# Performance work log

Measured on AMD Instinct MI355X. Metric: run time of the kernel, lower is better.

## Reference

```python
import jax, jax.numpy as jnp
import numpy as np

NUM_HEADS = 16
EMB = 1024
HEAD = 64
SEQ = 2048
BATCH = 4


def setup_inputs() -> dict:
    key = jax.random.key(0)
    ks = jax.random.split(key, 6)
    s = EMB ** -0.5
    x = jax.random.normal(ks[0], (BATCH, SEQ, EMB), dtype=jnp.float32)
    # per-head projection weights stacked: [H, E, D] (Linear(emb, head, bias=False) per head)
    Wq = jax.random.normal(ks[1], (NUM_HEADS, EMB, HEAD), dtype=jnp.float32) * s
    Wk = jax.random.normal(ks[2], (NUM_HEADS, EMB, HEAD), dtype=jnp.float32) * s
    Wv = jax.random.normal(ks[3], (NUM_HEADS, EMB, HEAD), dtype=jnp.float32) * s
    # output projection Linear(head*num_heads, emb): weight [E, H*D], bias [E]
    Wo = jax.random.normal(ks[4], (EMB, NUM_HEADS * HEAD), dtype=jnp.float32) * ((NUM_HEADS * HEAD) ** -0.5)
    bo = jax.random.normal(ks[5], (EMB,), dtype=jnp.float32) * 0.01
    return {"x": x, "Wq": Wq, "Wk": Wk, "Wv": Wv, "Wo": Wo, "bo": bo}


def reference(x, Wq, Wk, Wv, Wo, bo):
    B, S, E = x.shape
    scale = HEAD ** -0.5
    # batched per-head projections: [B, H, S, D]
    q = jnp.einsum('bse,hed->bhsd', x, Wq)
    k = jnp.einsum('bse,hed->bhsd', x, Wk)
    v = jnp.einsum('bse,hed->bhsd', x, Wv)
    scores = jnp.einsum('bhqd,bhkd->bhqk', q, k) * scale
    causal = jnp.tril(jnp.ones((S, S), dtype=bool))
    scores = jnp.where(causal, scores, jnp.finfo(scores.dtype).min)
    attn = jax.nn.softmax(scores, axis=-1)  # dropout disabled (eval/deterministic)
    ctx = jnp.einsum('bhqk,bhkd->bhqd', attn, v)
    # concat heads along last dim (head-major order, matching torch.cat)
    concat = ctx.transpose(0, 2, 1, 3).reshape(B, S, NUM_HEADS * HEAD)
    out = concat @ Wo.T + bo
    return out
```

## Files before the change

kernel.cpp:

```cpp
#include <hip/hip_runtime.h>

#define NHEADS 16
#define EMB 1024
#define HDIM 64
#define SEQ 2048
#define BATCH 4

typedef unsigned short u16;
typedef __attribute__((ext_vector_type(8))) __bf16 bf16x8;
typedef __attribute__((ext_vector_type(4))) float f32x4;

#if __has_builtin(__builtin_amdgcn_exp2f)
#define EXP2(x) __builtin_amdgcn_exp2f(x)
#else
#define EXP2(x) __expf((x)*0.69314718056f)
#endif
#define CL2E 0.18033688011112042f

#define BARRIER() __builtin_amdgcn_s_barrier()
#define SB0() __builtin_amdgcn_sched_barrier(0)
#define PRIO1() __builtin_amdgcn_s_setprio(1)
#define PRIO0() __builtin_amdgcn_s_setprio(0)
#define VMCNT(n) asm volatile("s_waitcnt vmcnt(" #n ")" ::: "memory")

__device__ __forceinline__ u16 f2bf(float f) {
  union { float f; unsigned u; } v; v.f = f;
  unsigned r = v.u + 0x7fffu + ((v.u >> 16) & 1u);
  return (u16)(r >> 16);
}
__device__ __forceinline__ unsigned pk2bf(float a, float b) {
  union { __bf16 h[2]; unsigned u; } x;
  x.h[0] = (__bf16)a; x.h[1] = (__bf16)b; return x.u;
}
__device__ __forceinline__ void gl16(const void* g, void* l) {
  __builtin_amdgcn_global_load_lds(
      (const __attribute__((address_space(1))) unsigned*)g,
      (__attribute__((address_space(3))) unsigned*)l, 16, 0, 0);
}

__global__ __launch_bounds__(256) void k_cvt(const float* __restrict__ in,
                                             u16* __restrict__ out, int n4) {
  int i = blockIdx.x * 256 + threadIdx.x;
  if (i >= n4) return;
  f32x4 v = *(const f32x4*)(in + (size_t)i * 4);
  uint2 o;
  o.x = (unsigned)f2bf(v[0]) | ((unsigned)f2bf(v[1]) << 16);
  o.y = (unsigned)f2bf(v[2]) | ((unsigned)f2bf(v[3]) << 16);
  *(uint2*)(out + (size_t)i * 4) = o;
}

__global__ __launch_bounds__(256) void k_packw(const float* __restrict__ Wq,
                                               const float* __restrict__ Wk,
                                               const float* __restrict__ Wv,
                                               u16* __restrict__ Wt) {
  const int mh = blockIdx.x;
  const int e0 = blockIdx.y * 64;
  const int mtx = mh >> 4, h = mh & 15;
  const float* W = (mtx == 0 ? Wq : (mtx == 1 ? Wk : Wv)) + (size_t)h * EMB * HDIM;
  __shared__ u16 sT[64][65];
  const int t = threadIdx.x;
  {
    int e = t >> 2, d0 = (t & 3) * 16;
#pragma unroll
    for (int jj = 0; jj < 4; jj++) {
      f32x4 v = *(const f32x4*)(W + (size_t)(e0 + e) * HDIM + d0 + jj * 4);
#pragma unroll
      for (int kk = 0; kk < 4; kk++) sT[e][d0 + jj * 4 + kk] = f2bf(v[kk]);
    }
  }
  __syncthreads();
  {
    int d = t >> 2, eb = (t & 3) * 16;
#pragma unroll
    for (int j = 0; j < 16; j++)
      Wt[(size_t)(mh * 64 + d) * EMB + e0 + eb + j] = sT[eb + j][d];
  }
}

__global__ __launch_bounds__(512, 2) void k_gemm_qkv8(const u16* __restrict__ Xb,
                                                      const u16* __restrict__ Wt,
                                                      u16* __restrict__ Q,
                                                      u16* __restrict__ K,
                                                      u16* __restrict__ V) {
  extern __shared__ __align__(16) char smem[];
  const int bid = blockIdx.x;
  const int l = (bid & 7) * 64 + (bid >> 3);
  const int mt = l & 31, nt = l >> 5;
  const int m0 = mt * 256, n0 = nt * 192;

  const int t = threadIdx.x;
  const int wave = t >> 6, lane = t & 63, lr = lane & 15, lg = lane >> 4;
  const int wr = (wave >> 2) * 128;
  const int wc = (wave & 3) * 48;

  const f32x4 fz = {0.f, 0.f, 0.f, 0.f};
  f32x4 acc[8][3];
#pragma unroll
  for (int i = 0; i < 8; i++)
#pragma unroll
    for (int j = 0; j < 3; j++) acc[i][j] = fz;

  bf16x8 af[4][2], bfr[3][2];

  auto SROUND = [&](char* ldsbase, int rbase, const u16* src, int gRowBase, int kt) {
    int rs = rbase + wave * 8;
    int row = rs + (lane >> 3);
    int gc = (lane & 7) ^ (row & 7);
    gl16(src + (size_t)(gRowBase + row) * EMB + kt * 64 + gc * 8, ldsbase + rs * 128);
  };
  auto LOADA = [&](const char* bA, int mh) {
#pragma unroll
    for (int mf = 0; mf < 4; mf++)
#pragma unroll
      for (int kf = 0; kf < 2; kf++) {
        int row = wr + mh * 64 + mf * 16 + lr;
        af[mf][kf] = *(const bf16x8*)(bA + row * 128 + ((kf * 64 + lg * 16) ^ ((row & 7) << 4)));
      }
  };
  auto LOADB = [&](const char* bB) {
#pragma unroll
    for (int nf = 0; nf < 3; nf++)
#pragma unroll
      for (int kf = 0; kf < 2; kf++) {
        int row = wc + nf * 16 + lr;
        bfr[nf][kf] = *(const bf16x8*)(bB + row * 128 + ((kf * 64 + lg * 16) ^ ((row & 7) << 4)));
      }
  };

#define MFMAPH(MH)                                                                         \
  do {                                                                                     \
    _Pragma("unroll") for (int kf = 0; kf < 2; kf++)                                       \
    _Pragma("unroll") for (int mf = 0; mf < 4; mf++)                                       \
    _Pragma("unroll") for (int nf = 0; nf < 3; nf++)                                       \
      acc[(MH)*4 + mf][nf] = __builtin_amdgcn_mfma_f32_16x16x32_bf16(                      \
          af[mf][kf], bfr[nf][kf], acc[(MH)*4 + mf][nf], 0, 0, 0);                         \
  } while (0)

  const int NT = EMB / 64;
  {
    char* nA = smem;
    char* nB = smem + 32768;
    SROUND(nB, 0, Wt, n0, 0); SROUND(nB, 64, Wt, n0, 0); SROUND(nB, 128, Wt, n0, 0);
    SROUND(nA, 0, Xb, m0, 0);
    SROUND(nA, 64, Xb, m0, 0); SROUND(nA, 128, Xb, m0, 0); SROUND(nA, 192, Xb, m0, 0);
  }
  VMCNT(0);
  BARRIER();

  for (int tt = 0; tt < NT - 1; tt++) {
    const int cb = tt & 1, nb = cb ^ 1;
    char* bA = smem + cb * 57344;
    char* bB = bA + 32768;
    char* nA = smem + nb * 57344;
    char* nB = nA + 32768;
    SROUND(nB, 0, Wt, n0, tt + 1);
    SROUND(nB, 64, Wt, n0, tt + 1);
    SROUND(nB, 128, Wt, n0, tt + 1);
    SROUND(nA, 0, Xb, m0, tt + 1);
    LOADA(bA, 0);
    LOADB(bB);
    VMCNT(4);
    BARRIER(); SB0();
    PRIO1(); MFMAPH(0); PRIO0();
    BARRIER();
    SROUND(nA, 64, Xb, m0, tt + 1);
    SROUND(nA, 128, Xb, m0, tt + 1);
    SROUND(nA, 192, Xb, m0, tt + 1);
    LOADA(bA, 1);
    VMCNT(2);
    BARRIER(); SB0();
    PRIO1(); MFMAPH(1); PRIO0();
    BARRIER();
  }
  {
    char* bA = smem + ((NT - 1) & 1) * 57344;
    char* bB = bA + 32768;
    LOADA(bA, 0);
    LOADB(bB);
    VMCNT(0);
    BARRIER(); SB0();
    PRIO1(); MFMAPH(0); PRIO0();
    LOADA(bA, 1);
    PRIO1(); MFMAPH(1); PRIO0();
  }
#undef MFMAPH

  const int b = m0 >> 11;
  const int s0 = m0 & 2047;
#pragma unroll
  for (int am = 0; am < 8; am++)
#pragma unroll
    for (int nf = 0; nf < 3; nf++)
#pragma unroll
      for (int r = 0; r < 4; r++) {
        int row = wr + am * 16 + lg * 4 + r;
        int n = n0 + wc + nf * 16 + lr;
        int mtx = n >> 10, h = (n >> 6) & 15, d = n & 63;
        u16* dst = (mtx == 0 ? Q : (mtx == 1 ? K : V));
        dst[((size_t)(b * NHEADS + h) * SEQ + s0 + row) * HDIM + d] = f2bf(acc[am][nf][r]);
      }
}

__global__ __launch_bounds__(256, 3) void k_attn(const u16* __restrict__ Q,
                                                 const u16* __restrict__ K,
                                                 const u16* __restrict__ V,
                                                 u16* __restrict__ Cc) {
  const int bh = blockIdx.x;
  const int qt = 15 - (int)blockIdx.y;
  const int b = bh >> 4, h = bh & 15;
  const int t = threadIdx.x;
  const int wq = t >> 6, lane = t & 63, lr = lane & 15, lg = lane >> 4;
  const size_t base = (size_t)bh * SEQ * HDIM;

  __shared__ __align__(16) char sK[64 * 128];
  __shared__ __align__(16) char sV[64 * 128];
  __shared__ __align__(16) char sP[128 * 128];

#pragma unroll
  for (int i = 0; i < 4; i++) {
    int rb = wq * 32 + i * 8;
    int row = rb + (lane >> 3);
    int gc = (lane & 7) ^ (row & 7);
    gl16(Q + base + (size_t)(qt * 128 + row) * HDIM + gc * 8, sP + rb * 128);
  }
  __syncthreads();
  bf16x8 qf[2][2];
#pragma unroll
  for (int q2 = 0; q2 < 2; q2++)
#pragma unroll
    for (int kf = 0; kf < 2; kf++) {
      int row = wq * 32 + q2 * 16 + lr;
      qf[q2][kf] = *(const bf16x8*)(sP + row * 128 + ((kf * 64 + lg * 16) ^ ((row & 7) << 4)));
    }

  const f32x4 fz = {0.f, 0.f, 0.f, 0.f};
  f32x4 ot[4][2];
#pragma unroll
  for (int df = 0; df < 4; df++)
#pragma unroll
    for (int q2 = 0; q2 < 2; q2++) ot[df][q2] = fz;
  float m_[2] = {-1e30f, -1e30f}, l_[2] = {0.f, 0.f};

  const int nsteps = 2 * qt + 2;
  for (int step = 0; step < nsteps; step++) {
    const int k0 = step * 64;
    __syncthreads();
#pragma unroll
    for (int i = 0; i < 2; i++) {
      int rb = wq * 16 + i * 8;
      int row = rb + (lane >> 3);
      int gc = (lane & 7) ^ (row & 7);
      gl16(K + base + (size_t)(k0 + row) * HDIM + gc * 8, sK + rb * 128);
    }
    {
      const int kv = lane, d0 = wq * 16;
      const u16* vp = V + base + (size_t)(k0 + kv) * HDIM + d0;
      bf16x8 v0 = *(const bf16x8*)vp;
      bf16x8 v1 = *(const bf16x8*)(vp + 8);
#pragma unroll
      for (int j = 0; j < 8; j++) {
        int d = d0 + j, d2 = d0 + 8 + j;
        *(__bf16*)(sV + d * 128 + ((kv * 2) ^ ((d & 7) << 4))) = v0[j];
        *(__bf16*)(sV + d2 * 128 + ((kv * 2) ^ ((d2 & 7) << 4))) = v1[j];
      }
    }
    __syncthreads();

    f32x4 st[4][2];
#pragma unroll
    for (int kvf = 0; kvf < 4; kvf++)
#pragma unroll
      for (int q2 = 0; q2 < 2; q2++) st[kvf][q2] = fz;
#pragma unroll
    for (int kf = 0; kf < 2; kf++) {
      bf16x8 kfr[4];
#pragma unroll
      for (int kvf = 0; kvf < 4; kvf++) {
        int row = kvf * 16 + lr;
        kfr[kvf] = *(const bf16x8*)(sK + row * 128 + ((kf * 64 + lg * 16) ^ ((row & 7) << 4)));
      }
#pragma unroll
      for (int kvf = 0; kvf < 4; kvf++)
#pragma unroll
        for (int q2 = 0; q2 < 2; q2++)
          st[kvf][q2] = __builtin_amdgcn_mfma_f32_16x16x32_bf16(kfr[kvf], qf[q2][kf], st[kvf][q2], 0, 0, 0);
    }

    const bool diag = (k0 >= qt * 128);
#pragma unroll
    for (int q2 = 0; q2 < 2; q2++) {
      if (diag) {
        const int qg = qt * 128 + wq * 32 + q2 * 16 + lr;
#pragma unroll
        for (int kvf = 0; kvf < 4; kvf++)
#pragma unroll
          for (int r = 0; r < 4; r++)
            if (k0 + kvf * 16 + 4 * lg + r > qg) st[kvf][q2][r] = -3e38f;
      }
      float mx = -3e38f;
#pragma unroll
      for (int kvf = 0; kvf < 4; kvf++)
        mx = fmaxf(mx, fmaxf(fmaxf(st[kvf][q2][0], st[kvf][q2][1]),
                             fmaxf(st[kvf][q2][2], st[kvf][q2][3])));
      mx = fmaxf(mx, __shfl_xor(mx, 16));
      mx = fmaxf(mx, __shfl_xor(mx, 32));
      float mnew = fmaxf(m_[q2], mx);
      float alpha = EXP2((m_[q2] - mnew) * CL2E);
      m_[q2] = mnew;
      float nmc = -mnew * CL2E;
      float rs = 0.f;
      const int prow = wq * 32 + q2 * 16 + lr;
#pragma unroll
      for (int kvf = 0; kvf < 4; kvf++) {
        float p0 = EXP2(fmaf(st[kvf][q2][0], CL2E, nmc));
        float p1 = EXP2(fmaf(st[kvf][q2][1], CL2E, nmc));
        float p2 = EXP2(fmaf(st[kvf][q2][2], CL2E, nmc));
        float p3 = EXP2(fmaf(st[kvf][q2][3], CL2E, nmc));
        rs += (p0 + p1) + (p2 + p3);
        uint2 w;
        w.x = pk2bf(p0, p1);
        w.y = pk2bf(p2, p3);
        *(uint2*)(sP + prow * 128 + ((kvf * 32 + lg * 8) ^ ((prow & 7) << 4))) = w;
      }
      rs += __shfl_xor(rs, 16);
      rs += __shfl_xor(rs, 32);
      l_[q2] = l_[q2] * alpha + rs;
#pragma unroll
      for (int df = 0; df < 4; df++) ot[df][q2] *= alpha;
    }

#pragma unroll
    for (int kf = 0; kf < 2; kf++) {
      bf16x8 pf[2], vf[4];
#pragma unroll
      for (int q2 = 0; q2 < 2; q2++) {
        int row = wq * 32 + q2 * 16 + lr;
        pf[q2] = *(const bf16x8*)(sP + row * 128 + ((kf * 64 + lg * 16) ^ ((row & 7) << 4)));
      }
#pragma unroll
      for (int df = 0; df < 4; df++) {
        int row = df * 16 + lr;
        vf[df] = *(const bf16x8*)(sV + row * 128 + ((kf * 64 + lg * 16) ^ ((row & 7) << 4)));
      }
#pragma unroll
      for (int df = 0; df < 4; df++)
#pragma unroll
        for (int q2 = 0; q2 < 2; q2++)
          ot[df][q2] = __builtin_amdgcn_mfma_f32_16x16x32_bf16(vf[df], pf[q2], ot[df][q2], 0, 0, 0);
    }
  }

#pragma unroll
  for (int q2 = 0; q2 < 2; q2++) {
    float inv = 1.0f / l_[q2];
    int s = qt * 128 + wq * 32 + q2 * 16 + lr;
#pragma unroll
    for (int df = 0; df < 4; df++) {
      uint2 w;
      w.x = pk2bf(ot[df][q2][0] * inv, ot[df][q2][1] * inv);
      w.y = pk2bf(ot[df][q2][2] * inv, ot[df][q2][3] * inv);
      *(uint2*)(Cc + ((size_t)b * SEQ + s) * (NHEADS * HDIM) + h * HDIM + df * 16 + 4 * lg) = w;
    }
  }
}

__global__ __launch_bounds__(256) void k_gemm_out(const u16* __restrict__ Cc,
                                                  const u16* __restrict__ Wob,
                                                  const float* __restrict__ bo,
                                                  float* __restrict__ out) {
  const int m0 = blockIdx.x * 128;
  const int n0 = blockIdx.y * 128;
  const int t = threadIdx.x;
  const int wave = t >> 6, lane = t & 63, lr = lane & 15, lg = lane >> 4;
  const int wr = (wave >> 1) * 64, wc = (wave & 1) * 64;

  __shared__ __align__(16) char sA[128 * 128];
  __shared__ __align__(16) char sB[128 * 128];

  const f32x4 fz = {0.f, 0.f, 0.f, 0.f};
  f32x4 acc[4][4];
#pragma unroll
  for (int i = 0; i < 4; i++)
#pragma unroll
    for (int j = 0; j < 4; j++) acc[i][j] = fz;

  for (int k0 = 0; k0 < EMB; k0 += 64) {
#pragma unroll
    for (int i = 0; i < 4; i++) {
      int rb = wave * 32 + i * 8;
      int row = rb + (lane >> 3);
      int gc = (lane & 7) ^ (row & 7);
      gl16(Cc + (size_t)(m0 + row) * EMB + k0 + gc * 8, sA + rb * 128);
      gl16(Wob + (size_t)(n0 + row) * EMB + k0 + gc * 8, sB + rb * 128);
    }
    __syncthreads();
    bf16x8 af[4][2], bfr[4][2];
#pragma unroll
    for (int mf = 0; mf < 4; mf++)
#pragma unroll
      for (int kf = 0; kf < 2; kf++) {
        int row = wr + mf * 16 + lr;
        af[mf][kf] = *(const bf16x8*)(sA + row * 128 + ((kf * 64 + lg * 16) ^ ((row & 7) << 4)));
      }
#pragma unroll
    for (int nf = 0; nf < 4; nf++)
#pragma unroll
      for (int kf = 0; kf < 2; kf++) {
        int row = wc + nf * 16 + lr;
        bfr[nf][kf] = *(const bf16x8*)(sB + row * 128 + ((kf * 64 + lg * 16) ^ ((row & 7) << 4)));
      }
#pragma unroll
    for (int kf = 0; kf < 2; kf++)
#pragma unroll
      for (int mf = 0; mf < 4; mf++)
#pragma unroll
        for (int nf = 0; nf < 4; nf++)
          acc[mf][nf] = __builtin_amdgcn_mfma_f32_16x16x32_bf16(af[mf][kf], bfr[nf][kf], acc[mf][nf], 0, 0, 0);
    __syncthreads();
  }

  float bv[4];
#pragma unroll
  for (int nf = 0; nf < 4; nf++) bv[nf] = bo[n0 + wc + nf * 16 + lr];
#pragma unroll
  for (int mf = 0; mf < 4; mf++)
#pragma unroll
    for (int nf = 0; nf < 4; nf++)
#pragma unroll
      for (int r = 0; r < 4; r++) {
        int row = wr + mf * 16 + lg * 4 + r;
        int n = n0 + wc + nf * 16 + lr;
        out[(size_t)(m0 + row) * EMB + n] = acc[mf][nf][r] + bv[nf];
      }
}

extern "C" void kernel_launch(void* const* d_in, const int* in_sizes, int n_in,
                              void* d_out, int out_size, void* d_ws, size_t ws_size,
                              hipStream_t stream) {
  const float* x  = (const float*)d_in[0];
  const float* Wq = (const float*)d_in[1];
  const float* Wk = (const float*)d_in[2];
  const float* Wv = (const float*)d_in[3];
  const float* Wo = (const float*)d_in[4];
  const float* bo = (const float*)d_in[5];
  float* out = (float*)d_out;

  char* ws = (char*)d_ws;
  const size_t SZ_XB  = (size_t)8192 * 1024 * 2;
  const size_t SZ_WT  = (size_t)3072 * 1024 * 2;
  const size_t SZ_WOB = (size_t)1024 * 1024 * 2;
  const size_t SZ_QKV = (size_t)64 * 2048 * 64 * 2;
  u16* Xb  = (u16*)(ws);
  u16* Wt  = (u16*)(ws + SZ_XB);
  u16* Wob = (u16*)(ws + SZ_XB + SZ_WT);
  u16* Qb  = (u16*)(ws + SZ_XB + SZ_WT + SZ_WOB);
  u16* Kb  = (u16*)(ws + SZ_XB + SZ_WT + SZ_WOB + SZ_QKV);
  u16* Vb  = (u16*)(ws + SZ_XB + SZ_WT + SZ_WOB + 2 * SZ_QKV);
  u16* Cc  = (u16*)(ws + SZ_XB + SZ_WT + SZ_WOB + 3 * SZ_QKV);

  k_cvt<<<8192, 256, 0, stream>>>(x, Xb, 2097152);
  k_cvt<<<1024, 256, 0, stream>>>(Wo, Wob, 262144);
  k_packw<<<dim3(48, 16), 256, 0, stream>>>(Wq, Wk, Wv, Wt);
  k_gemm_qkv8<<<512, 512, 114688, stream>>>(Xb, Wt, Qb, Kb, Vb);
  k_attn<<<dim3(64, 16), 256, 0, stream>>>(Qb, Kb, Vb, Cc);
  k_gemm_out<<<dim3(64, 8), 256, 0, stream>>>(Cc, Wob, bo, out);
}
```

Measured before the change: 172.2 us.

## Add lazy softmax rescale, vectorized V transpose, and raise attention occupancy hint

The online softmax now skips the running-max update and the rescaling of the output accumulators unless some row's new max exceeds the stored max by more than a threshold (wave-uniform check). The V tile transpose into shared memory uses 4x4 bf16 blocks built with byte-permute instructions and 8-byte LDS stores, replacing scalar 2-byte stores. The launch bounds minimum-blocks hint for the attention kernel goes from 3 to 5, which can force register spilling. The lazy rescale lets exponentials grow up to 2^(64*log2e) before renormalizing, which relies on fp32 headroom and bf16 P values.

```diff
diff --git a/kernel.cpp b/kernel.cpp
--- a/kernel.cpp
+++ b/kernel.cpp
@@ -36,6 +36,12 @@
   __builtin_amdgcn_global_load_lds(
       (const __attribute__((address_space(1))) unsigned*)g,
       (__attribute__((address_space(3))) unsigned*)l, 16, 0, 0);
+}
+__device__ __forceinline__ unsigned PKLO(unsigned a, unsigned b) {
+  return __builtin_amdgcn_perm(a, b, 0x01000504u);
+}
+__device__ __forceinline__ unsigned PKHI(unsigned a, unsigned b) {
+  return __builtin_amdgcn_perm(a, b, 0x03020706u);
 }
 
 __global__ __launch_bounds__(256) void k_cvt(const float* __restrict__ in,
@@ -201,7 +207,7 @@
       }
 }
 
-__global__ __launch_bounds__(256, 3) void k_attn(const u16* __restrict__ Q,
+__global__ __launch_bounds__(256, 5) void k_attn(const u16* __restrict__ Q,
                                                  const u16* __restrict__ K,
                                                  const u16* __restrict__ V,
                                                  u16* __restrict__ Cc) {
@@ -253,16 +259,20 @@
       gl16(K + base + (size_t)(k0 + row) * HDIM + gc * 8, sK + rb * 128);
     }
     {
-      const int kv = lane, d0 = wq * 16;
-      const u16* vp = V + base + (size_t)(k0 + kv) * HDIM + d0;
-      bf16x8 v0 = *(const bf16x8*)vp;
-      bf16x8 v1 = *(const bf16x8*)(vp + 8);
-#pragma unroll
-      for (int j = 0; j < 8; j++) {
-        int d = d0 + j, d2 = d0 + 8 + j;
-        *(__bf16*)(sV + d * 128 + ((kv * 2) ^ ((d & 7) << 4))) = v0[j];
-        *(__bf16*)(sV + d2 * 128 + ((kv * 2) ^ ((d2 & 7) << 4))) = v1[j];
-      }
+      const int kvb = (t & 15) * 4, db = (t >> 4) * 4;
+      const u16* vp = V + base + (size_t)(k0 + kvb) * HDIM + db;
+      uint2 v0 = *(const uint2*)(vp);
+      uint2 v1 = *(const uint2*)(vp + HDIM);
+      uint2 v2 = *(const uint2*)(vp + 2 * HDIM);
+      uint2 v3 = *(const uint2*)(vp + 3 * HDIM);
+      uint2 w0 = {PKLO(v0.x, v1.x), PKLO(v2.x, v3.x)};
+      uint2 w1 = {PKHI(v0.x, v1.x), PKHI(v2.x, v3.x)};
+      uint2 w2 = {PKLO(v0.y, v1.y), PKLO(v2.y, v3.y)};
+      uint2 w3 = {PKHI(v0.y, v1.y), PKHI(v2.y, v3.y)};
+      *(uint2*)(sV + (db + 0) * 128 + ((kvb * 2) ^ (((db + 0) & 7) << 4))) = w0;
+      *(uint2*)(sV + (db + 1) * 128 + ((kvb * 2) ^ (((db + 1) & 7) << 4))) = w1;
+      *(uint2*)(sV + (db + 2) * 128 + ((kvb * 2) ^ (((db + 2) & 7) << 4))) = w2;
+      *(uint2*)(sV + (db + 3) * 128 + ((kvb * 2) ^ (((db + 3) & 7) << 4))) = w3;
     }
     __syncthreads();
 
@@ -287,6 +297,7 @@
     }
 
     const bool diag = (k0 >= qt * 128);
+    float mxv[2];
 #pragma unroll
     for (int q2 = 0; q2 < 2; q2++) {
       if (diag) {
@@ -304,10 +315,22 @@
                              fmaxf(st[kvf][q2][2], st[kvf][q2][3])));
       mx = fmaxf(mx, __shfl_xor(mx, 16));
       mx = fmaxf(mx, __shfl_xor(mx, 32));
-      float mnew = fmaxf(m_[q2], mx);
-      float alpha = EXP2((m_[q2] - mnew) * CL2E);
-      m_[q2] = mnew;
-      float nmc = -mnew * CL2E;
+      mxv[q2] = mx;
+    }
+    if (!__all((mxv[0] <= m_[0] + 64.f) && (mxv[1] <= m_[1] + 64.f))) {
+#pragma unroll
+      for (int q2 = 0; q2 < 2; q2++) {
+        float mnew = fmaxf(m_[q2], mxv[q2]);
+        float alpha = EXP2((m_[q2] - mnew) * CL2E);
+        m_[q2] = mnew;
+        l_[q2] *= alpha;
+#pragma unroll
+        for (int df = 0; df < 4; df++) ot[df][q2] *= alpha;
+      }
+    }
+#pragma unroll
+    for (int q2 = 0; q2 < 2; q2++) {
+      float nmc = -m_[q2] * CL2E;
       float rs = 0.f;
       const int prow = wq * 32 + q2 * 16 + lr;
 #pragma unroll
@@ -324,9 +347,7 @@
       }
       rs += __shfl_xor(rs, 16);
       rs += __shfl_xor(rs, 32);
-      l_[q2] = l_[q2] * alpha + rs;
-#pragma unroll
-      for (int df = 0; df < 4; df++) ot[df][q2] *= alpha;
+      l_[q2] += rs;
     }
 
 #pragma unroll
```

Result: slower. 333.9 us (+93.9%).
